# Performance work log

Hardware: AMD Instinct MI355X
Metric: run time of the kernel (lower is better)

## Reference

```python
import jax, jax.numpy as jnp
import numpy as np

N = 50000
E = 800000


def gcn_conv(x, row, col, dinv_sqrt, W, b, n_nodes):
    # PyG GCNConv: x' = lin(x); out[col] += norm * x'[row]; out += bias
    # norm = dinv_sqrt[row] * dinv_sqrt[col] (self-loops already in row/col)
    xw = x @ W                                  # [N, out_dim]
    norm = dinv_sqrt[row] * dinv_sqrt[col]      # [E']
    msg = xw[row] * norm[:, None]               # [E', out_dim]
    out = jax.ops.segment_sum(msg, col, num_segments=n_nodes)
    return out + b


def setup_inputs() -> dict:
    key = jax.random.key(0)
    k1, k2, k3, k4 = jax.random.split(key, 4)
    x = jax.random.normal(k1, (N, 128), dtype=jnp.float32)
    edge_index = jax.random.randint(k2, (2, E), 0, N, dtype=jnp.int64)
    W1 = jax.random.normal(k3, (128, 64), dtype=jnp.float32) * (1.0 / np.sqrt(128))
    b1 = jnp.zeros((64,), dtype=jnp.float32)
    W2 = jax.random.normal(k4, (64, 32), dtype=jnp.float32) * (1.0 / np.sqrt(64))
    b2 = jnp.zeros((32,), dtype=jnp.float32)
    return {"x": x, "edge_index": edge_index, "W1": W1, "b1": b1, "W2": W2, "b2": b2}


def reference(x, edge_index, W1, b1, W2, b2):
    n_nodes = x.shape[0]
    # add self loops (fixed size -> jit friendly)
    loops = jnp.arange(n_nodes, dtype=edge_index.dtype)
    row = jnp.concatenate([edge_index[0], loops])  # source
    col = jnp.concatenate([edge_index[1], loops])  # target
    # symmetric normalization from in-degree (all edge weights = 1)
    deg = jax.ops.segment_sum(jnp.ones_like(col, dtype=x.dtype), col, num_segments=n_nodes)
    dinv_sqrt = jnp.where(deg > 0, jax.lax.rsqrt(deg), 0.0)

    h = gcn_conv(x, row, col, dinv_sqrt, W1, b1, n_nodes)
    h = jax.nn.relu(h)
    h = gcn_conv(h, row, col, dinv_sqrt, W2, b2, n_nodes)
    return jax.nn.log_softmax(h, axis=1)
```

## Files before the change

kernel.cpp:

```cpp
#include <hip/hip_runtime.h>

#define F0 128
#define F1 64
#define F2 32
#define CPB 256
#define EPB 4096

typedef unsigned short ushort_t;
typedef unsigned int uint_t;

__device__ __forceinline__ ushort_t f2bf(float f) {
    uint_t u = __float_as_uint(f);
    return (ushort_t)((u + 0x7FFFu + ((u >> 16) & 1u)) >> 16);
}
__device__ __forceinline__ float bf2f(ushort_t u) {
    return __uint_as_float((uint_t)u << 16);
}

__global__ void zero_b(int* __restrict__ bcnt) {
    bcnt[threadIdx.x] = 0;
}

__global__ __launch_bounds__(256) void bucket_count(const int* __restrict__ col,
                                                    int* __restrict__ bcnt, int E) {
    __shared__ int h[256];
    int t = threadIdx.x;
    h[t] = 0;
    __syncthreads();
    int e0 = blockIdx.x * EPB;
    int cnt = E - e0; if (cnt > EPB) cnt = EPB;
    for (int k = t; k < cnt; k += 256) atomicAdd(&h[col[e0 + k] >> 8], 1);
    __syncthreads();
    if (h[t]) atomicAdd(&bcnt[t], h[t]);
}

__global__ __launch_bounds__(256) void bucket_scan(const int* __restrict__ bcnt,
                                                   int* __restrict__ bucket_base,
                                                   int* __restrict__ cur2) {
    __shared__ int s[256];
    int t = threadIdx.x;
    int v = bcnt[t];
    s[t] = v;
    __syncthreads();
    for (int off = 1; off < 256; off <<= 1) {
        int u = (t >= off) ? s[t - off] : 0;
        __syncthreads();
        s[t] += u;
        __syncthreads();
    }
    int p = s[t] - v;
    bucket_base[t] = p;
    cur2[t] = p;
}

__global__ __launch_bounds__(256) void coarse_part(const int* __restrict__ row,
                                                   const int* __restrict__ col,
                                                   int* cur2, uint_t* __restrict__ ebuf,
                                                   int E) {
    __shared__ uint_t stage[EPB];
    __shared__ int hist[256];
    __shared__ int hbase[256];
    int t = threadIdx.x;
    int e0 = blockIdx.x * EPB;
    int cnt = E - e0; if (cnt > EPB) cnt = EPB;
    hist[t] = 0;
    __syncthreads();
    for (int k = t; k < cnt; k += 256) {
        int c = col[e0 + k], r = row[e0 + k];
        stage[k] = ((uint_t)r << 16) | (uint_t)c;
        atomicAdd(&hist[c >> 8], 1);
    }
    __syncthreads();
    int h = hist[t];
    if (h > 0) hbase[t] = atomicAdd(&cur2[t], h);
    __syncthreads();
    hist[t] = 0;
    __syncthreads();
    for (int k = t; k < cnt; k += 256) {
        uint_t p = stage[k];
        int b = (int)((p & 0xFFFFu) >> 8);
        int rk = atomicAdd(&hist[b], 1);
        ebuf[hbase[b] + rk] = p;
    }
}

__global__ __launch_bounds__(256) void fine_build(const int* __restrict__ bucket_base,
                                                  const uint_t* __restrict__ ebuf,
                                                  int* __restrict__ ptr,
                                                  float* __restrict__ dinv,
                                                  int* __restrict__ erow,
                                                  int N, int E, int nbuck) {
    __shared__ int hist[CPB];
    __shared__ int pref[CPB];
    int b = blockIdx.x;
    int cbase = b << 8;
    int t = threadIdx.x;
    int seg0 = bucket_base[b];
    int seg1 = (b + 1 < nbuck) ? bucket_base[b + 1] : E;
    hist[t] = 0;
    __syncthreads();
    for (int k = seg0 + t; k < seg1; k += 256)
        atomicAdd(&hist[ebuf[k] & 255u], 1);
    __syncthreads();
    int deg = hist[t];
    pref[t] = deg;
    __syncthreads();
    for (int off = 1; off < 256; off <<= 1) {
        int u = (t >= off) ? pref[t - off] : 0;
        __syncthreads();
        pref[t] += u;
        __syncthreads();
    }
    int base = seg0 + pref[t] - deg;
    int c = cbase + t;
    if (c < N) {
        ptr[c] = base;
        dinv[c] = rsqrtf((float)(deg + 1));
    }
    if (b == nbuck - 1 && t == 0) ptr[N] = E;
    __syncthreads();
    pref[t] = base;
    __syncthreads();
    for (int k = seg0 + t; k < seg1; k += 256) {
        uint_t p = ebuf[k];
        int pos = atomicAdd(&pref[p & 255u], 1);
        erow[pos] = (int)(p >> 16);
    }
}

__device__ __forceinline__ void fma4(float4& a, float xs, const float4& wv) {
    a.x = fmaf(xs, wv.x, a.x);
    a.y = fmaf(xs, wv.y, a.y);
    a.z = fmaf(xs, wv.z, a.z);
    a.w = fmaf(xs, wv.w, a.w);
}

__global__ __launch_bounds__(256) void gemm1(const float* __restrict__ x,
                                             const float* __restrict__ W,
                                             const float* __restrict__ dinv,
                                             ushort_t* __restrict__ xwb, int N) {
    __shared__ float Xl[64 * F0];
    __shared__ float Wl[F0 * F1];
    int tid = threadIdx.x;
    int base = blockIdx.x * 64;

    const float4* W4 = (const float4*)W;
    float4* Wl4 = (float4*)Wl;
#pragma unroll
    for (int i = 0; i < 8; ++i) Wl4[tid + 256 * i] = W4[tid + 256 * i];

    float4* Xl4 = (float4*)Xl;
#pragma unroll
    for (int i = 0; i < 8; ++i) {
        int idx = tid + 256 * i;
        int r = idx >> 5, c4 = idx & 31;
        int gr = base + r;
        float4 v = (gr < N) ? ((const float4*)x)[(size_t)gr * 32 + c4]
                            : make_float4(0.f, 0.f, 0.f, 0.f);
        Xl4[r * 32 + (c4 ^ (r >> 2))] = v;
    }
    __syncthreads();

    int tc = tid & 15, tr = tid >> 4;
    float4 acc0 = make_float4(0.f, 0.f, 0.f, 0.f);
    float4 acc1 = acc0, acc2 = acc0, acc3 = acc0;
    const float4* Wl4c = (const float4*)Wl;
    const float4* Xl4c = (const float4*)Xl;

#pragma unroll 4
    for (int kk = 0; kk < 32; ++kk) {
        float4 xv0 = Xl4c[(4 * tr + 0) * 32 + (kk ^ tr)];
        float4 xv1 = Xl4c[(4 * tr + 1) * 32 + (kk ^ tr)];
        float4 xv2 = Xl4c[(4 * tr + 2) * 32 + (kk ^ tr)];
        float4 xv3 = Xl4c[(4 * tr + 3) * 32 + (kk ^ tr)];
        float4 w0 = Wl4c[(4 * kk + 0) * 16 + tc];
        float4 w1 = Wl4c[(4 * kk + 1) * 16 + tc];
        float4 w2 = Wl4c[(4 * kk + 2) * 16 + tc];
        float4 w3 = Wl4c[(4 * kk + 3) * 16 + tc];
        fma4(acc0, xv0.x, w0); fma4(acc0, xv0.y, w1); fma4(acc0, xv0.z, w2); fma4(acc0, xv0.w, w3);
        fma4(acc1, xv1.x, w0); fma4(acc1, xv1.y, w1); fma4(acc1, xv1.z, w2); fma4(acc1, xv1.w, w3);
        fma4(acc2, xv2.x, w0); fma4(acc2, xv2.y, w1); fma4(acc2, xv2.z, w2); fma4(acc2, xv2.w, w3);
        fma4(acc3, xv3.x, w0); fma4(acc3, xv3.y, w1); fma4(acc3, xv3.z, w2); fma4(acc3, xv3.w, w3);
    }

    int gr = base + 4 * tr;
#pragma unroll
    for (int k = 0; k < 4; ++k) {
        int r = gr + k;
        if (r < N) {
            float d = dinv[r];
            float4 a = (k == 0) ? acc0 : (k == 1) ? acc1 : (k == 2) ? acc2 : acc3;
            ushort4 o = make_ushort4(f2bf(a.x * d), f2bf(a.y * d), f2bf(a.z * d), f2bf(a.w * d));
            *(ushort4*)(&xwb[(size_t)r * F1 + 4 * tc]) = o;
        }
    }
}

__global__ void agg1(const int* __restrict__ ptr, const int* __restrict__ erow,
                     const ushort_t* __restrict__ xwb, const float* __restrict__ dinv,
                     const float* __restrict__ b, ushort_t* __restrict__ h1b, int N) {
    int t = blockIdx.x * 256 + threadIdx.x;
    int i = t >> 6, j = t & 63;
    if (i >= N) return;
    float acc = bf2f(xwb[(size_t)i * F1 + j]);
    int e = ptr[i], end = ptr[i + 1];
    while (e < end && (e & 3)) {
        acc += bf2f(xwb[(size_t)erow[e] * F1 + j]);
        ++e;
    }
    for (; e + 7 < end; e += 8) {
        int4 a4 = *(const int4*)&erow[e];
        int4 b4 = *(const int4*)&erow[e + 4];
        float v0 = bf2f(xwb[(size_t)a4.x * F1 + j]);
        float v1 = bf2f(xwb[(size_t)a4.y * F1 + j]);
        float v2 = bf2f(xwb[(size_t)a4.z * F1 + j]);
        float v3 = bf2f(xwb[(size_t)a4.w * F1 + j]);
        float v4 = bf2f(xwb[(size_t)b4.x * F1 + j]);
        float v5 = bf2f(xwb[(size_t)b4.y * F1 + j]);
        float v6 = bf2f(xwb[(size_t)b4.z * F1 + j]);
        float v7 = bf2f(xwb[(size_t)b4.w * F1 + j]);
        acc += v0; acc += v1; acc += v2; acc += v3;
        acc += v4; acc += v5; acc += v6; acc += v7;
    }
    if (e + 3 < end) {
        int4 a4 = *(const int4*)&erow[e];
        acc += bf2f(xwb[(size_t)a4.x * F1 + j]);
        acc += bf2f(xwb[(size_t)a4.y * F1 + j]);
        acc += bf2f(xwb[(size_t)a4.z * F1 + j]);
        acc += bf2f(xwb[(size_t)a4.w * F1 + j]);
        e += 4;
    }
    for (; e < end; ++e) acc += bf2f(xwb[(size_t)erow[e] * F1 + j]);
    h1b[(size_t)i * F1 + j] = f2bf(fmaxf(acc * dinv[i] + b[j], 0.0f));
}

__global__ __launch_bounds__(256) void gemm2(const ushort_t* __restrict__ h1b,
                                             const float* __restrict__ W,
                                             const float* __restrict__ dinv,
                                             ushort_t* __restrict__ hwb, int N) {
    __shared__ float Hl[128 * F1];
    __shared__ float Wl[F1 * F2];
    int tid = threadIdx.x;
    int base = blockIdx.x * 128;

    const float4* W4 = (const float4*)W;
    float4* Wl4 = (float4*)Wl;
#pragma unroll
    for (int i = 0; i < 2; ++i) Wl4[tid + 256 * i] = W4[tid + 256 * i];

    const uint4* H4 = (const uint4*)h1b;
    float4* Hl4 = (float4*)Hl;
#pragma unroll
    for (int it = 0; it < 4; ++it) {
        int g = tid + 256 * it;
        int r = g >> 3, c8 = g & 7;
        int gr = base + r;
        uint4 v = (gr < N) ? H4[(size_t)gr * 8 + c8] : make_uint4(0, 0, 0, 0);
        float4 a, b2;
        a.x = bf2f((ushort_t)(v.x & 0xFFFF)); a.y = bf2f((ushort_t)(v.x >> 16));
        a.z = bf2f((ushort_t)(v.y & 0xFFFF)); a.w = bf2f((ushort_t)(v.y >> 16));
        b2.x = bf2f((ushort_t)(v.z & 0xFFFF)); b2.y = bf2f((ushort_t)(v.z >> 16));
        b2.z = bf2f((ushort_t)(v.w & 0xFFFF)); b2.w = bf2f((ushort_t)(v.w >> 16));
        int sw = (r >> 2) & 15;
        Hl4[r * 16 + ((2 * c8 + 0) ^ sw)] = a;
        Hl4[r * 16 + ((2 * c8 + 1) ^ sw)] = b2;
    }
    __syncthreads();

    int tc = tid & 7, tr = tid >> 3;
    float4 acc0 = make_float4(0.f, 0.f, 0.f, 0.f);
    float4 acc1 = acc0, acc2 = acc0, acc3 = acc0;
    const float4* Wl4c = (const float4*)Wl;
    const float4* Hl4c = (const float4*)Hl;

#pragma unroll 4
    for (int kk = 0; kk < 16; ++kk) {
        int sw = kk ^ (tr & 15);
        float4 xv0 = Hl4c[(4 * tr + 0) * 16 + sw];
        float4 xv1 = Hl4c[(4 * tr + 1) * 16 + sw];
        float4 xv2 = Hl4c[(4 * tr + 2) * 16 + sw];
        float4 xv3 = Hl4c[(4 * tr + 3) * 16 + sw];
        float4 w0 = Wl4c[(4 * kk + 0) * 8 + tc];
        float4 w1 = Wl4c[(4 * kk + 1) * 8 + tc];
        float4 w2 = Wl4c[(4 * kk + 2) * 8 + tc];
        float4 w3 = Wl4c[(4 * kk + 3) * 8 + tc];
        fma4(acc0, xv0.x, w0); fma4(acc0, xv0.y, w1); fma4(acc0, xv0.z, w2); fma4(acc0, xv0.w, w3);
        fma4(acc1, xv1.x, w0); fma4(acc1, xv1.y, w1); fma4(acc1, xv1.z, w2); fma4(acc1, xv1.w, w3);
        fma4(acc2, xv2.x, w0); fma4(acc2, xv2.y, w1); fma4(acc2, xv2.z, w2); fma4(acc2, xv2.w, w3);
        fma4(acc3, xv3.x, w0); fma4(acc3, xv3.y, w1); fma4(acc3, xv3.z, w2); fma4(acc3, xv3.w, w3);
    }

    int gr = base + 4 * tr;
#pragma unroll
    for (int k = 0; k < 4; ++k) {
        int r = gr + k;
        if (r < N) {
            float d = dinv[r];
            float4 a = (k == 0) ? acc0 : (k == 1) ? acc1 : (k == 2) ? acc2 : acc3;
            ushort4 o = make_ushort4(f2bf(a.x * d), f2bf(a.y * d), f2bf(a.z * d), f2bf(a.w * d));
            *(ushort4*)(&hwb[(size_t)r * F2 + 4 * tc]) = o;
        }
    }
}

__global__ void agg2_lsm(const int* __restrict__ ptr, const int* __restrict__ erow,
                         const ushort_t* __restrict__ hwb, const float* __restrict__ dinv,
                         const float* __restrict__ b, float* __restrict__ out, int N) {
    int t = blockIdx.x * 256 + threadIdx.x;
    int i = t >> 5, j = t & 31;
    if (i >= N) return;
    float acc = bf2f(hwb[(size_t)i * F2 + j]);
    int e = ptr[i], end = ptr[i + 1];
    while (e < end && (e & 3)) {
        acc += bf2f(hwb[(size_t)erow[e] * F2 + j]);
        ++e;
    }
    for (; e + 7 < end; e += 8) {
        int4 a4 = *(const int4*)&erow[e];
        int4 b4 = *(const int4*)&erow[e + 4];
        float v0 = bf2f(hwb[(size_t)a4.x * F2 + j]);
        float v1 = bf2f(hwb[(size_t)a4.y * F2 + j]);
        float v2 = bf2f(hwb[(size_t)a4.z * F2 + j]);
        float v3 = bf2f(hwb[(size_t)a4.w * F2 + j]);
        float v4 = bf2f(hwb[(size_t)b4.x * F2 + j]);
        float v5 = bf2f(hwb[(size_t)b4.y * F2 + j]);
        float v6 = bf2f(hwb[(size_t)b4.z * F2 + j]);
        float v7 = bf2f(hwb[(size_t)b4.w * F2 + j]);
        acc += v0; acc += v1; acc += v2; acc += v3;
        acc += v4; acc += v5; acc += v6; acc += v7;
    }
    if (e + 3 < end) {
        int4 a4 = *(const int4*)&erow[e];
        acc += bf2f(hwb[(size_t)a4.x * F2 + j]);
        acc += bf2f(hwb[(size_t)a4.y * F2 + j]);
        acc += bf2f(hwb[(size_t)a4.z * F2 + j]);
        acc += bf2f(hwb[(size_t)a4.w * F2 + j]);
        e += 4;
    }
    for (; e < end; ++e) acc += bf2f(hwb[(size_t)erow[e] * F2 + j]);
    acc = acc * dinv[i] + b[j];
    float m = acc;
    for (int off = 16; off; off >>= 1) m = fmaxf(m, __shfl_xor(m, off, 32));
    float s = expf(acc - m);
    for (int off = 16; off; off >>= 1) s += __shfl_xor(s, off, 32);
    out[(size_t)i * F2 + j] = acc - m - logf(s);
}

extern "C" void kernel_launch(void* const* d_in, const int* in_sizes, int n_in,
                              void* d_out, int out_size, void* d_ws, size_t ws_size,
                              hipStream_t stream) {
    const float* x  = (const float*)d_in[0];
    const int*   ei = (const int*)d_in[1];
    const float* W1 = (const float*)d_in[2];
    const float* b1 = (const float*)d_in[3];
    const float* W2 = (const float*)d_in[4];
    const float* b2 = (const float*)d_in[5];

    int N = in_sizes[0] / F0;
    int E = in_sizes[1] / 2;
    const int* row = ei;
    const int* col = ei + E;

    size_t Np = ((size_t)N + 63) & ~(size_t)63;
    size_t Ep = ((size_t)E + 63) & ~(size_t)63;
    int*      bcnt        = (int*)d_ws;
    int*      bucket_base = bcnt + 256;
    int*      cur2        = bucket_base + 256;
    int*      ptr         = cur2 + 256 + 64;
    float*    dinv        = (float*)(ptr + Np + 64);
    int*      erow        = (int*)(dinv + Np);
    uint_t*   ebuf        = (uint_t*)(erow + Ep);
    ushort_t* xwb         = (ushort_t*)(ebuf + Ep);
    ushort_t* h1b         = xwb + Np * F1;
    ushort_t* hwb         = h1b + Np * F1;
    float*    out2        = (float*)d_out;

    int nbC   = (E + EPB - 1) / EPB;
    int nbuck = (N + CPB - 1) / CPB;

    zero_b<<<1, 256, 0, stream>>>(bcnt);
    bucket_count<<<nbC, 256, 0, stream>>>(col, bcnt, E);
    bucket_scan<<<1, 256, 0, stream>>>(bcnt, bucket_base, cur2);
    coarse_part<<<nbC, 256, 0, stream>>>(row, col, cur2, ebuf, E);
    fine_build<<<nbuck, 256, 0, stream>>>(bucket_base, ebuf, ptr, dinv, erow, N, E, nbuck);

    gemm1<<<(N + 63) / 64, 256, 0, stream>>>(x, W1, dinv, xwb, N);
    agg1<<<(int)(((size_t)N * F1 + 255) / 256), 256, 0, stream>>>(ptr, erow, xwb, dinv, b1, h1b, N);
    gemm2<<<(N + 127) / 128, 256, 0, stream>>>(h1b, W2, dinv, hwb, N);
    agg2_lsm<<<(int)(((size_t)N * F2 + 255) / 256), 256, 0, stream>>>(ptr, erow, hwb, dinv, b2, out2, N);
}
```

Before: 129.1 us.

## Pack bf16 pairs per lane and split edges across half-wavefronts in aggregation

The aggregation kernels now have each lane load a 32-bit word holding two bf16 features. Each half of the node's lane group walks alternate edges, and the two partial sums are combined with a shuffle. Edge source indices are stored as 16-bit values, which halves index traffic but only holds while N fits in 16 bits. The log-softmax reduction now works on two values per lane across 16 lanes. The aim is fewer, wider gathers and more edge-level parallelism per node, at the cost of a cross-half shuffle and idle lanes at the final store.

Result: faster. 120.9 us (-6.4%).

```diff
diff --git a/kernel.cpp b/kernel.cpp
--- a/kernel.cpp
+++ b/kernel.cpp
@@ -16,6 +16,8 @@
 __device__ __forceinline__ float bf2f(ushort_t u) {
     return __uint_as_float((uint_t)u << 16);
 }
+__device__ __forceinline__ float bflo(uint_t v) { return __uint_as_float(v << 16); }
+__device__ __forceinline__ float bfhi(uint_t v) { return __uint_as_float(v & 0xFFFF0000u); }
 
 __global__ void zero_b(int* __restrict__ bcnt) {
     bcnt[threadIdx.x] = 0;
@@ -88,7 +90,7 @@
                                                   const uint_t* __restrict__ ebuf,
                                                   int* __restrict__ ptr,
                                                   float* __restrict__ dinv,
-                                                  int* __restrict__ erow,
+                                                  ushort_t* __restrict__ erow,
                                                   int N, int E, int nbuck) {
     __shared__ int hist[CPB];
     __shared__ int pref[CPB];
@@ -124,7 +126,7 @@
     for (int k = seg0 + t; k < seg1; k += 256) {
         uint_t p = ebuf[k];
         int pos = atomicAdd(&pref[p & 255u], 1);
-        erow[pos] = (int)(p >> 16);
+        erow[pos] = (ushort_t)(p >> 16);
     }
 }
 
@@ -196,42 +198,49 @@
     }
 }
 
-__global__ void agg1(const int* __restrict__ ptr, const int* __restrict__ erow,
+__global__ void agg1(const int* __restrict__ ptr, const ushort_t* __restrict__ erow,
                      const ushort_t* __restrict__ xwb, const float* __restrict__ dinv,
                      const float* __restrict__ b, ushort_t* __restrict__ h1b, int N) {
     int t = blockIdx.x * 256 + threadIdx.x;
-    int i = t >> 6, j = t & 63;
+    int i = t >> 6;
     if (i >= N) return;
-    float acc = bf2f(xwb[(size_t)i * F1 + j]);
+    int l = t & 63, h = l >> 5, l2 = l & 31;
+    const uint_t* xwb2 = (const uint_t*)xwb;
+
+    float a0 = 0.f, a1 = 0.f;
     int e = ptr[i], end = ptr[i + 1];
-    while (e < end && (e & 3)) {
-        acc += bf2f(xwb[(size_t)erow[e] * F1 + j]);
-        ++e;
-    }
     for (; e + 7 < end; e += 8) {
-        int4 a4 = *(const int4*)&erow[e];
-        int4 b4 = *(const int4*)&erow[e + 4];
-        float v0 = bf2f(xwb[(size_t)a4.x * F1 + j]);
-        float v1 = bf2f(xwb[(size_t)a4.y * F1 + j]);
-        float v2 = bf2f(xwb[(size_t)a4.z * F1 + j]);
-        float v3 = bf2f(xwb[(size_t)a4.w * F1 + j]);
-        float v4 = bf2f(xwb[(size_t)b4.x * F1 + j]);
-        float v5 = bf2f(xwb[(size_t)b4.y * F1 + j]);
-        float v6 = bf2f(xwb[(size_t)b4.z * F1 + j]);
-        float v7 = bf2f(xwb[(size_t)b4.w * F1 + j]);
-        acc += v0; acc += v1; acc += v2; acc += v3;
-        acc += v4; acc += v5; acc += v6; acc += v7;
-    }
-    if (e + 3 < end) {
-        int4 a4 = *(const int4*)&erow[e];
-        acc += bf2f(xwb[(size_t)a4.x * F1 + j]);
-        acc += bf2f(xwb[(size_t)a4.y * F1 + j]);
-        acc += bf2f(xwb[(size_t)a4.z * F1 + j]);
-        acc += bf2f(xwb[(size_t)a4.w * F1 + j]);
-        e += 4;
-    }
-    for (; e < end; ++e) acc += bf2f(xwb[(size_t)erow[e] * F1 + j]);
-    h1b[(size_t)i * F1 + j] = f2bf(fmaxf(acc * dinv[i] + b[j], 0.0f));
+        int r0 = erow[e + 0 + h], r1 = erow[e + 2 + h];
+        int r2 = erow[e + 4 + h], r3 = erow[e + 6 + h];
+        uint_t v0 = xwb2[(size_t)r0 * 32 + l2];
+        uint_t v1 = xwb2[(size_t)r1 * 32 + l2];
+        uint_t v2 = xwb2[(size_t)r2 * 32 + l2];
+        uint_t v3 = xwb2[(size_t)r3 * 32 + l2];
+        a0 += bflo(v0); a1 += bfhi(v0);
+        a0 += bflo(v1); a1 += bfhi(v1);
+        a0 += bflo(v2); a1 += bfhi(v2);
+        a0 += bflo(v3); a1 += bfhi(v3);
+    }
+    for (; e + 1 < end; e += 2) {
+        int r0 = erow[e + h];
+        uint_t v0 = xwb2[(size_t)r0 * 32 + l2];
+        a0 += bflo(v0); a1 += bfhi(v0);
+    }
+    if (e < end && h == 0) {
+        uint_t v0 = xwb2[(size_t)erow[e] * 32 + l2];
+        a0 += bflo(v0); a1 += bfhi(v0);
+    }
+    a0 += __shfl_down(a0, 32, 64);
+    a1 += __shfl_down(a1, 32, 64);
+    if (h == 0) {
+        uint_t sv = xwb2[(size_t)i * 32 + l2];
+        a0 += bflo(sv); a1 += bfhi(sv);
+        float d = dinv[i];
+        float2 bb = ((const float2*)b)[l2];
+        a0 = fmaxf(a0 * d + bb.x, 0.f);
+        a1 = fmaxf(a1 * d + bb.y, 0.f);
+        ((uint_t*)h1b)[(size_t)i * 32 + l2] = (uint_t)f2bf(a0) | ((uint_t)f2bf(a1) << 16);
+    }
 }
 
 __global__ __launch_bounds__(256) void gemm2(const ushort_t* __restrict__ h1b,
@@ -257,10 +266,10 @@
         int gr = base + r;
         uint4 v = (gr < N) ? H4[(size_t)gr * 8 + c8] : make_uint4(0, 0, 0, 0);
         float4 a, b2;
-        a.x = bf2f((ushort_t)(v.x & 0xFFFF)); a.y = bf2f((ushort_t)(v.x >> 16));
-        a.z = bf2f((ushort_t)(v.y & 0xFFFF)); a.w = bf2f((ushort_t)(v.y >> 16));
-        b2.x = bf2f((ushort_t)(v.z & 0xFFFF)); b2.y = bf2f((ushort_t)(v.z >> 16));
-        b2.z = bf2f((ushort_t)(v.w & 0xFFFF)); b2.w = bf2f((ushort_t)(v.w >> 16));
+        a.x = bflo(v.x); a.y = bfhi(v.x);
+        a.z = bflo(v.y); a.w = bfhi(v.y);
+        b2.x = bflo(v.z); b2.y = bfhi(v.z);
+        b2.z = bflo(v.w); b2.w = bfhi(v.w);
         int sw = (r >> 2) & 15;
         Hl4[r * 16 + ((2 * c8 + 0) ^ sw)] = a;
         Hl4[r * 16 + ((2 * c8 + 1) ^ sw)] = b2;
@@ -303,47 +312,55 @@
     }
 }
 
-__global__ void agg2_lsm(const int* __restrict__ ptr, const int* __restrict__ erow,
+__global__ void agg2_lsm(const int* __restrict__ ptr, const ushort_t* __restrict__ erow,
                          const ushort_t* __restrict__ hwb, const float* __restrict__ dinv,
                          const float* __restrict__ b, float* __restrict__ out, int N) {
     int t = blockIdx.x * 256 + threadIdx.x;
-    int i = t >> 5, j = t & 31;
+    int i = t >> 5;
     if (i >= N) return;
-    float acc = bf2f(hwb[(size_t)i * F2 + j]);
+    int g = t & 31, h = g >> 4, l2 = g & 15;
+    const uint_t* hwb2 = (const uint_t*)hwb;
+
+    float a0 = 0.f, a1 = 0.f;
     int e = ptr[i], end = ptr[i + 1];
-    while (e < end && (e & 3)) {
-        acc += bf2f(hwb[(size_t)erow[e] * F2 + j]);
-        ++e;
-    }
     for (; e + 7 < end; e += 8) {
-        int4 a4 = *(const int4*)&erow[e];
-        int4 b4 = *(const int4*)&erow[e + 4];
-        float v0 = bf2f(hwb[(size_t)a4.x * F2 + j]);
-        float v1 = bf2f(hwb[(size_t)a4.y * F2 + j]);
-        float v2 = bf2f(hwb[(size_t)a4.z * F2 + j]);
-        float v3 = bf2f(hwb[(size_t)a4.w * F2 + j]);
-        float v4 = bf2f(hwb[(size_t)b4.x * F2 + j]);
-        float v5 = bf2f(hwb[(size_t)b4.y * F2 + j]);
-        float v6 = bf2f(hwb[(size_t)b4.z * F2 + j]);
-        float v7 = bf2f(hwb[(size_t)b4.w * F2 + j]);
-        acc += v0; acc += v1; acc += v2; acc += v3;
-        acc += v4; acc += v5; acc += v6; acc += v7;
-    }
-    if (e + 3 < end) {
-        int4 a4 = *(const int4*)&erow[e];
-        acc += bf2f(hwb[(size_t)a4.x * F2 + j]);
-        acc += bf2f(hwb[(size_t)a4.y * F2 + j]);
-        acc += bf2f(hwb[(size_t)a4.z * F2 + j]);
-        acc += bf2f(hwb[(size_t)a4.w * F2 + j]);
-        e += 4;
-    }
-    for (; e < end; ++e) acc += bf2f(hwb[(size_t)erow[e] * F2 + j]);
-    acc = acc * dinv[i] + b[j];
-    float m = acc;
-    for (int off = 16; off; off >>= 1) m = fmaxf(m, __shfl_xor(m, off, 32));
-    float s = expf(acc - m);
-    for (int off = 16; off; off >>= 1) s += __shfl_xor(s, off, 32);
-    out[(size_t)i * F2 + j] = acc - m - logf(s);
+        int r0 = erow[e + 0 + h], r1 = erow[e + 2 + h];
+        int r2 = erow[e + 4 + h], r3 = erow[e + 6 + h];
+        uint_t v0 = hwb2[(size_t)r0 * 16 + l2];
+        uint_t v1 = hwb2[(size_t)r1 * 16 + l2];
+        uint_t v2 = hwb2[(size_t)r2 * 16 + l2];
+        uint_t v3 = hwb2[(size_t)r3 * 16 + l2];
+        a0 += bflo(v0); a1 += bfhi(v0);
+        a0 += bflo(v1); a1 += bfhi(v1);
+        a0 += bflo(v2); a1 += bfhi(v2);
+        a0 += bflo(v3); a1 += bfhi(v3);
+    }
+    for (; e + 1 < end; e += 2) {
+        int r0 = erow[e + h];
+        uint_t v0 = hwb2[(size_t)r0 * 16 + l2];
+        a0 += bflo(v0); a1 += bfhi(v0);
+    }
+    if (e < end && h == 0) {
+        uint_t v0 = hwb2[(size_t)erow[e] * 16 + l2];
+        a0 += bflo(v0); a1 += bfhi(v0);
+    }
+    a0 += __shfl_down(a0, 16, 32);
+    a1 += __shfl_down(a1, 16, 32);
+
+    uint_t sv = hwb2[(size_t)i * 16 + l2];
+    a0 += bflo(sv); a1 += bfhi(sv);
+    float d = dinv[i];
+    float2 bb = ((const float2*)b)[l2];
+    a0 = a0 * d + bb.x;
+    a1 = a1 * d + bb.y;
+
+    float m = fmaxf(a0, a1);
+    for (int off = 8; off; off >>= 1) m = fmaxf(m, __shfl_xor(m, off, 16));
+    float s = expf(a0 - m) + expf(a1 - m);
+    for (int off = 8; off; off >>= 1) s += __shfl_xor(s, off, 16);
+    float ls = logf(s);
+    if (h == 0)
+        ((float2*)out)[(size_t)i * 16 + l2] = make_float2(a0 - m - ls, a1 - m - ls);
 }
 
 extern "C" void kernel_launch(void* const* d_in, const int* in_sizes, int n_in,
@@ -368,7 +385,7 @@
     int*      cur2        = bucket_base + 256;
     int*      ptr         = cur2 + 256 + 64;
     float*    dinv        = (float*)(ptr + Np + 64);
-    int*      erow        = (int*)(dinv + Np);
+    ushort_t* erow        = (ushort_t*)(dinv + Np);
     uint_t*   ebuf        = (uint_t*)(erow + Ep);
     ushort_t* xwb         = (ushort_t*)(ebuf + Ep);
     ushort_t* h1b         = xwb + Np * F1;
@@ -385,7 +402,7 @@
     fine_build<<<nbuck, 256, 0, stream>>>(bucket_base, ebuf, ptr, dinv, erow, N, E, nbuck);
 
     gemm1<<<(N + 63) / 64, 256, 0, stream>>>(x, W1, dinv, xwb, N);
-    agg1<<<(int)(((size_t)N * F1 + 255) / 256), 256, 0, stream>>>(ptr, erow, xwb, dinv, b1, h1b, N);
+    agg1<<<(int)(((size_t)N * 64 + 255) / 256), 256, 0, stream>>>(ptr, erow, xwb, dinv, b1, h1b, N);
     gemm2<<<(N + 127) / 128, 256, 0, stream>>>(h1b, W2, dinv, hwb, N);
-    agg2_lsm<<<(int)(((size_t)N * F2 + 255) / 256), 256, 0, stream>>>(ptr, erow, hwb, dinv, b2, out2, N);
-}
+    agg2_lsm<<<(int)(((size_t)N * 32 + 255) / 256), 256, 0, stream>>>(ptr, erow, hwb, dinv, b2, out2, N);
+}
```
